# Optimization experiments

Measured on AMD Instinct MI355X. Metric: run time of the kernel, lower is better.

## Reference

```python
import jax, jax.numpy as jnp
import numpy as np

N, E, G = 2048, 4096, 128      # nodes, edges, graphs
H, IN, ED = 128, 11, 4         # hidden, input node feat, edge feat
BN_EPS = 1e-5


def setup_inputs() -> dict:
    key = jax.random.key(0)
    ks = iter(jax.random.split(key, 40))
    r = lambda shape, s=0.1: jax.random.normal(next(ks), shape, jnp.float32) * s
    inp = dict(
        x=r((N, IN), 1.0),
        edge_attr=jax.random.uniform(next(ks), (E, ED), jnp.float32),
        edge_index=jax.random.randint(next(ks), (2, E), 0, N).astype(jnp.int32),
        batch=jnp.sort(jax.random.randint(next(ks), (N,), 0, G)).astype(jnp.int32),
        # layer 0 (in=11 -> out=128)
        w1_0=r((ED, H)), b1_0=jnp.zeros(H), w2_0=r((H, IN * H), 0.02), b2_0=jnp.zeros(IN * H),
        root_0=r((IN, H)), bias_0=jnp.zeros(H),
        bn_g0=jnp.ones(H), bn_b0=jnp.zeros(H), bn_m0=r((H,), 0.1),
        bn_v0=jax.random.uniform(next(ks), (H,), jnp.float32, 0.5, 1.5),
        # layers 1..4 stacked (in=out=128)
        w1_s=r((4, ED, H)), b1_s=jnp.zeros((4, H)), w2_s=r((4, H, H * H), 0.02), b2_s=jnp.zeros((4, H * H)),
        root_s=r((4, H, H)), bias_s=jnp.zeros((4, H)),
        bn_gs=jnp.ones((4, H)), bn_bs=jnp.zeros((4, H)), bn_ms=r((4, H), 0.1),
        bn_vs=jax.random.uniform(next(ks), (4, H), jnp.float32, 0.5, 1.5),
        # readout MLP
        lin1_w=r((H, H // 2)), lin1_b=jnp.zeros(H // 2),
        lin2_w=r((H // 2, 1)), lin2_b=jnp.zeros(1),
    )
    return inp


def _nnconv(x, src, dst, edge_attr, w1, b1, w2, b2, root, bias):
    in_c = x.shape[-1]
    h = jax.nn.relu(edge_attr @ w1 + b1)                 # [E, H]
    w_e = (h @ w2 + b2).reshape(-1, in_c, H)             # [E, in, H] per-edge weight
    msg = jnp.einsum('ei,eio->eo', x[src], w_e)          # gather + per-edge matvec
    s = jax.ops.segment_sum(msg, dst, num_segments=N)
    cnt = jax.ops.segment_sum(jnp.ones(dst.shape, x.dtype), dst, num_segments=N)
    aggr = s / jnp.maximum(cnt, 1.0)[:, None]            # scatter-mean
    return aggr + x @ root + bias


def _bn_eval(x, g, b, m, v):
    return (x - m) * jax.lax.rsqrt(v + BN_EPS) * g + b


def reference(x, edge_attr, w1_0, b1_0, w2_0, b2_0, root_0, bias_0,
              bn_g0, bn_b0, bn_m0, bn_v0,
              w1_s, b1_s, w2_s, b2_s, root_s, bias_s,
              bn_gs, bn_bs, bn_ms, bn_vs,
              lin1_w, lin1_b, lin2_w, lin2_b,
              edge_index, batch):
    src, dst = edge_index[0], edge_index[1]
    # layer 0
    h = jax.nn.relu(_bn_eval(
        _nnconv(x, src, dst, edge_attr, w1_0, b1_0, w2_0, b2_0, root_0, bias_0),
        bn_g0, bn_b0, bn_m0, bn_v0))
    # layers 1..4 with residual (dims match)
    for l in range(4):
        h_new = jax.nn.relu(_bn_eval(
            _nnconv(h, src, dst, edge_attr, w1_s[l], b1_s[l], w2_s[l], b2_s[l], root_s[l], bias_s[l]),
            bn_gs[l], bn_bs[l], bn_ms[l], bn_vs[l]))
        h = h + h_new
    # global mean pool over graphs
    gs = jax.ops.segment_sum(h, batch, num_segments=G)
    gc = jax.ops.segment_sum(jnp.ones((N,), h.dtype), batch, num_segments=G)
    g = gs / jnp.maximum(gc, 1.0)[:, None]
    # readout (dropout is identity in eval mode)
    g = jax.nn.relu(g @ lin1_w + lin1_b)
    return g @ lin2_w + lin2_b
```

## Files before the change

### kernel.cpp

```cpp
#include <hip/hip_runtime.h>
#include <cstdint>
#include <cstddef>

#define NN 2048
#define NE 4096
#define NG 128
#define HD 128
#define SKM 16
#define SK0 5
#define NCH 64
#define CHE 64

typedef __attribute__((ext_vector_type(8))) _Float16 f16x8;
typedef __attribute__((ext_vector_type(4))) float f32x4;

#define GLOAD_LDS16(gptr, lptr)                                                          \
  __builtin_amdgcn_global_load_lds((const __attribute__((address_space(1))) unsigned int*)(gptr), \
                                   (__attribute__((address_space(3))) unsigned int*)(lptr), 16, 0, 0)

__global__ __launch_bounds__(256) void k_prep(
    const float* __restrict__ ea,
    const float* __restrict__ w1_0, const float* __restrict__ b1_0,
    const float* __restrict__ w1_s, const float* __restrict__ b1_s,
    const float* __restrict__ x,
    const float* __restrict__ w2_0, const float* __restrict__ b2_0,
    const float* __restrict__ w2s, const float* __restrict__ b2s,
    const int* __restrict__ dst, int* __restrict__ hist,
    _Float16* __restrict__ hb, _Float16* __restrict__ x16,
    _Float16* __restrict__ w2T0, _Float16* __restrict__ w2T) {
  __shared__ float s[64][65];
  const int bid = blockIdx.x, t = threadIdx.x;

  if (bid < 10240) {
    int idx = bid * 256 + t;
    int c = idx & (HD - 1);
    int e = (idx >> 7) & (NE - 1);
    int l = idx >> 19;
    const float* w1 = (l == 0) ? w1_0 : (w1_s + (size_t)(l - 1) * 4 * HD);
    const float* b1 = (l == 0) ? b1_0 : (b1_s + (size_t)(l - 1) * HD);
    float4 a = *(const float4*)(ea + (size_t)e * 4);
    float v = b1[c] + a.x * w1[c] + a.y * w1[HD + c] + a.z * w1[2 * HD + c] + a.w * w1[3 * HD + c];
    hb[idx] = (_Float16)fmaxf(v, 0.f);
  } else if (bid < 10368) {
    int idx = (bid - 10240) * 256 + t;
    int n = idx >> 4, i = idx & 15;
    x16[idx] = (_Float16)(i < 11 ? x[(size_t)n * 11 + i] : 0.f);
  } else if (bid < 10496) {
    int o = bid - 10368;
    for (int kap = t; kap < 2080; kap += 256) {
      int k = kap >> 4, i = kap & 15;
      float v = 0.f;
      if (i < 11) {
        if (k < 128) v = w2_0[(size_t)k * 1408 + i * 128 + o];
        else if (k == 128) v = b2_0[i * 128 + o];
      }
      w2T0[(size_t)o * 2080 + kap] = (_Float16)v;
    }
  } else if (bid < 12560) {
    int idx2 = bid - 10496;
    int l = idx2 / 516;
    int rem = idx2 - l * 516;
    int ob = rem / 258;
    int kb = rem - ob * 258;
    const float* w2 = w2s + (size_t)l * 16384 * 128;
    const float* b2 = b2s + (size_t)l * 128 * 128;
    _Float16* out = w2T + (size_t)l * 128 * 16512;
    int k0 = kb * 64, o0 = ob * 64;
    int r = t >> 4, c4 = (t & 15) * 4;
#pragma unroll
    for (int it = 0; it < 4; ++it) {
      int kk = k0 + r + it * 16;
      const float* srcp = (kk < 16384) ? (w2 + (size_t)kk * 128 + o0 + c4)
                                       : (b2 + (size_t)(kk - 16384) * 128 + o0 + c4);
      *(float4*)&s[r + it * 16][c4] = *(const float4*)srcp;
    }
    __syncthreads();
    int rr = t >> 3, c8 = (t & 7) * 8;
#pragma unroll
    for (int it = 0; it < 2; ++it) {
      int ol = rr + it * 32;
      _Float16 pk[8];
#pragma unroll
      for (int j = 0; j < 8; ++j) pk[j] = (_Float16)s[c8 + j][ol];
      *(f16x8*)(out + (size_t)(o0 + ol) * 16512 + k0 + c8) = *(const f16x8*)pk;
    }
  } else {
    int e = (bid - 12560) * 256 + t;
    if (e < NE) atomicAdd(&hist[(e >> 6) * NN + dst[e]], 1);
  }
}

__global__ __launch_bounds__(1024) void k_scan2(const int* __restrict__ hist,
                                                int* __restrict__ rowptr,
                                                int* __restrict__ chunkoff,
                                                const int* __restrict__ batch,
                                                int* __restrict__ gstart) {
  __shared__ int s[NN];
  int t = threadIdx.x;
  int c0 = 0, c1 = 0;
  for (int c = 0; c < NCH; ++c) { c0 += hist[c * NN + t]; c1 += hist[c * NN + t + 1024]; }
  s[t] = c0; s[t + 1024] = c1;
  __syncthreads();
  for (int d = 1; d < NN; d <<= 1) {
    int a0 = s[t], a1 = s[t + 1024];
    int v0 = (t >= d) ? s[t - d] : 0;
    int v1 = (t + 1024 >= d) ? s[t + 1024 - d] : 0;
    __syncthreads();
    s[t] = a0 + v0; s[t + 1024] = a1 + v1;
    __syncthreads();
  }
  rowptr[t + 1] = s[t]; rowptr[t + 1025] = s[t + 1024];
  if (t == 0) rowptr[0] = 0;
  int run0 = s[t] - c0, run1 = s[t + 1024] - c1;
  for (int c = 0; c < NCH; ++c) {
    chunkoff[c * NN + t] = run0;        run0 += hist[c * NN + t];
    chunkoff[c * NN + t + 1024] = run1; run1 += hist[c * NN + t + 1024];
  }
  if (t <= NG) {
    int lo = 0, hi = NN;
    while (lo < hi) { int mid = (lo + hi) >> 1; if (batch[mid] < t) lo = mid + 1; else hi = mid; }
    gstart[t] = lo;
  }
}

__global__ __launch_bounds__(64) void k_fill2(const int* __restrict__ dst,
                                              const int* __restrict__ chunkoff,
                                              int* __restrict__ elist) {
  __shared__ int sd[CHE];
  int c = blockIdx.x, t = threadIdx.x;
  int e = c * CHE + t;
  int dv = dst[e];
  sd[t] = dv;
  __syncthreads();
  int lrank = 0;
  for (int j = 0; j < t; ++j) lrank += (sd[j] == dv) ? 1 : 0;
  elist[chunkoff[c * NN + dv] + lrank] = e;
}

__global__ __launch_bounds__(256, 2) void k_mma0(
    const _Float16* __restrict__ xh,
    const _Float16* __restrict__ hb,
    const _Float16* __restrict__ w2T,
    const int* __restrict__ src,
    _Float16* __restrict__ msgp) {
  constexpr int KT = 2080;
  __shared__ _Float16 Bs[2][4096];
  __shared__ _Float16 hTl[26][128];

  const int tid = threadIdx.x;
  const int e0 = blockIdx.x * 128;
  const int w = tid >> 6, l = tid & 63, l16 = l & 15, g = l >> 4;

  const int k0 = blockIdx.y * 13, nk = 13;
  const int kb = k0 * 2;

  int nd[8];
#pragma unroll
  for (int mt = 0; mt < 8; ++mt) nd[mt] = src[e0 + mt * 16 + l16];

  for (int idx = tid; idx < 26 * 128; idx += 256) {
    int kk = idx >> 7, m = idx & 127;
    int k = kb + kk;
    _Float16 v;
    if (k < 128) v = hb[(size_t)(e0 + m) * 128 + k];
    else v = (k == 128) ? (_Float16)1.0f : (_Float16)0.0f;
    hTl[kk][m] = v;
  }

  f16x8 xr[8];
#pragma unroll
  for (int mt = 0; mt < 8; ++mt)
    xr[mt] = *(const f16x8*)(xh + (size_t)nd[mt] * 16 + (g & 1) * 8);

  auto stageB = [&](int buf, int c) {
    const int kap0 = c * 32;
#pragma unroll
    for (int j2 = 0; j2 < 2; ++j2) {
      int ntg = w * 2 + j2;
      const _Float16* gp = w2T + (size_t)(ntg * 16 + l16) * KT + kap0 + g * 8;
      GLOAD_LDS16(gp, &Bs[buf][(w * 128 + j2 * 64) * 8]);
    }
  };

  stageB(0, k0);
  __syncthreads();

  f32x4 acc[8][2];
#pragma unroll
  for (int mt = 0; mt < 8; ++mt)
#pragma unroll
    for (int jj = 0; jj < 2; ++jj) acc[mt][jj] = (f32x4){0.f, 0.f, 0.f, 0.f};

  int buf = 0;
  for (int j = 0; j < nk; ++j) {
    if (j + 1 < nk) {
      stageB(buf ^ 1, k0 + j + 1);
      asm volatile("s_waitcnt vmcnt(2)" ::: "memory");
    } else {
      asm volatile("s_waitcnt vmcnt(0)" ::: "memory");
    }
    __builtin_amdgcn_sched_barrier(0);

    f16x8 bv0 = *(const f16x8*)&Bs[buf][(size_t)(w * 2 + 0) * 512 + l * 8];
    f16x8 bv1 = *(const f16x8*)&Bs[buf][(size_t)(w * 2 + 1) * 512 + l * 8];
#pragma unroll
    for (int mt = 0; mt < 8; ++mt) {
      _Float16 hh = hTl[2 * j + (g >> 1)][mt * 16 + l16];
      f16x8 hv = {hh, hh, hh, hh, hh, hh, hh, hh};
      f16x8 av = xr[mt] * hv;
      acc[mt][0] = __builtin_amdgcn_mfma_f32_16x16x32_f16(av, bv0, acc[mt][0], 0, 0, 0);
      acc[mt][1] = __builtin_amdgcn_mfma_f32_16x16x32_f16(av, bv1, acc[mt][1], 0, 0, 0);
    }
    buf ^= 1;
    __syncthreads();
  }

  _Float16* mp = msgp + ((size_t)blockIdx.y * NE + e0) * 128;
#pragma unroll
  for (int mt = 0; mt < 8; ++mt)
#pragma unroll
    for (int jj = 0; jj < 2; ++jj)
#pragma unroll
      for (int r = 0; r < 4; ++r) {
        int row = mt * 16 + 4 * g + r;
        mp[(size_t)row * 128 + w * 32 + jj * 16 + l16] = (_Float16)acc[mt][jj][r];
      }
}

__global__ __launch_bounds__(512, 2) void k_mma3(
    const _Float16* __restrict__ xh,
    const _Float16* __restrict__ hb,
    const _Float16* __restrict__ w2T,
    const int* __restrict__ src,
    _Float16* __restrict__ msgp) {
  constexpr int KT = 16512;
  __shared__ __align__(16) _Float16 Bs[4][4096];
  __shared__ _Float16 hTl[9][256];

  const int tid = threadIdx.x;
  const int w = tid >> 6, l = tid & 63, l16 = l & 15, g = l >> 4;
  const int bid = blockIdx.x;
  const int eb = bid >> 4, sk = bid & 15;
  const int e0 = eb * 256;
  const int mg = w & 3, ng = w >> 2;

  int k0, nk;
  if (sk == 0) { k0 = 0; nk = 9; } else { k0 = 9 + (sk - 1) * 8; nk = 8; }
  const int nsteps = nk * 4;

  auto stageB = [&](int s) {
    const int jk = s >> 2, win = s & 3;
    const int kap0 = (k0 + jk) * 128 + win * 32;
    const _Float16* gp = w2T + (size_t)(w * 16 + l16) * KT + kap0 + g * 8;
    GLOAD_LDS16(gp, &Bs[s & 3][w * 512]);
  };

  stageB(0);
  stageB(1);

  int nd[4];
#pragma unroll
  for (int mt = 0; mt < 4; ++mt) nd[mt] = src[e0 + mg * 64 + mt * 16 + l16];
  f16x8 xw[4][4];
#pragma unroll
  for (int mt = 0; mt < 4; ++mt)
#pragma unroll
    for (int win = 0; win < 4; ++win)
      xw[mt][win] = *(const f16x8*)(xh + (size_t)nd[mt] * 128 + win * 32 + g * 8);

  for (int idx = tid; idx < nk * 256; idx += 512) {
    int jk = idx >> 8, m = idx & 255;
    int k = k0 + jk;
    hTl[jk][m] = (k < 128) ? hb[(size_t)(e0 + m) * 128 + k]
                           : (_Float16)(k == 128 ? 1.0f : 0.0f);
  }
  __syncthreads();

  f32x4 acc[4][4];
#pragma unroll
  for (int mt = 0; mt < 4; ++mt)
#pragma unroll
    for (int j2 = 0; j2 < 4; ++j2) acc[mt][j2] = (f32x4){0.f, 0.f, 0.f, 0.f};

  for (int jk = 0; jk < nk; ++jk) {
    _Float16 hv[4];
#pragma unroll
    for (int mt = 0; mt < 4; ++mt) hv[mt] = hTl[jk][mg * 64 + mt * 16 + l16];
#pragma unroll
    for (int win = 0; win < 4; ++win) {
      const int s = jk * 4 + win;
      if (s + 2 < nsteps) {
        stageB(s + 2);
        asm volatile("s_waitcnt vmcnt(2)" ::: "memory");
      } else if (s + 2 == nsteps) {
        asm volatile("s_waitcnt vmcnt(1)" ::: "memory");
      } else {
        asm volatile("s_waitcnt vmcnt(0)" ::: "memory");
      }
      __builtin_amdgcn_s_barrier();

      const _Float16* bp = &Bs[win][ng * 2048 + g * 128 + l16 * 8];
      f16x8 bv0 = *(const f16x8*)(bp);
      f16x8 bv1 = *(const f16x8*)(bp + 512);
      f16x8 bv2 = *(const f16x8*)(bp + 1024);
      f16x8 bv3 = *(const f16x8*)(bp + 1536);
#pragma unroll
      for (int mt = 0; mt < 4; ++mt) {
        _Float16 hh = hv[mt];
        f16x8 hs = {hh, hh, hh, hh, hh, hh, hh, hh};
        f16x8 av = xw[mt][win] * hs;
        acc[mt][0] = __builtin_amdgcn_mfma_f32_16x16x32_f16(av, bv0, acc[mt][0], 0, 0, 0);
        acc[mt][1] = __builtin_amdgcn_mfma_f32_16x16x32_f16(av, bv1, acc[mt][1], 0, 0, 0);
        acc[mt][2] = __builtin_amdgcn_mfma_f32_16x16x32_f16(av, bv2, acc[mt][2], 0, 0, 0);
        acc[mt][3] = __builtin_amdgcn_mfma_f32_16x16x32_f16(av, bv3, acc[mt][3], 0, 0, 0);
      }
    }
  }

  _Float16* mp = msgp + ((size_t)sk * NE + e0) * 128;
#pragma unroll
  for (int mt = 0; mt < 4; ++mt)
#pragma unroll
    for (int j2 = 0; j2 < 4; ++j2)
#pragma unroll
      for (int r = 0; r < 4; ++r) {
        int row = mg * 64 + mt * 16 + 4 * g + r;
        int col = (ng * 4 + j2) * 16 + l16;
        mp[(size_t)row * 128 + col] = (_Float16)acc[mt][j2][r];
      }
}

template <int INR, int NSK>
__global__ void k_au(const _Float16* __restrict__ msgp, const int* __restrict__ rowptr,
                     const int* __restrict__ elist, const float* __restrict__ xin,
                     const float* __restrict__ root, const float* __restrict__ bias,
                     const float* __restrict__ bg, const float* __restrict__ bb,
                     const float* __restrict__ bm, const float* __restrict__ bv,
                     const float* __restrict__ h_prev, float* __restrict__ h_out,
                     _Float16* __restrict__ h_out_h) {
  int n = blockIdx.x, t = threadIdx.x;
  __shared__ float xr[INR];
  if (t < INR) xr[t] = xin[(size_t)n * INR + t];
  int beg = rowptr[n], end = rowptr[n + 1];
  float v = 0.f;
  for (int j = beg; j < end; ++j) {
    int e = elist[j];
#pragma unroll
    for (int s = 0; s < NSK; ++s) v += (float)msgp[((size_t)s * NE + e) * HD + t];
  }
  v /= fmaxf((float)(end - beg), 1.f);
  __syncthreads();
  float acc = v + bias[t];
#pragma unroll 8
  for (int k = 0; k < INR; ++k) acc += xr[k] * root[(size_t)k * HD + t];
  float bn = (acc - bm[t]) * rsqrtf(bv[t] + 1e-5f) * bg[t] + bb[t];
  float r = fmaxf(bn, 0.f);
  float val = h_prev ? (h_prev[(size_t)n * HD + t] + r) : r;
  h_out[(size_t)n * HD + t] = val;
  h_out_h[(size_t)n * HD + t] = (_Float16)val;
}

__global__ void k_poolread(const float* __restrict__ h, const int* __restrict__ gstart,
                           const float* __restrict__ w1, const float* __restrict__ b1,
                           const float* __restrict__ w2, const float* __restrict__ b2,
                           float* __restrict__ out) {
  int g = blockIdx.x, t = threadIdx.x;
  __shared__ float row[HD];
  int beg = gstart[g], end = gstart[g + 1];
  float v = 0.f;
  for (int n = beg; n < end; ++n) v += h[(size_t)n * HD + t];
  row[t] = v / fmaxf((float)(end - beg), 1.f);
  __syncthreads();
  if (t < 64) {
    float acc = b1[t];
#pragma unroll 8
    for (int k = 0; k < HD; ++k) acc += row[k] * w1[(size_t)k * 64 + t];
    float vv = fmaxf(acc, 0.f) * w2[t];
#pragma unroll
    for (int off = 32; off > 0; off >>= 1) vv += __shfl_down(vv, off);
    if (t == 0) out[g] = vv + b2[0];
  }
}

extern "C" void kernel_launch(void* const* d_in, const int* in_sizes, int n_in,
                              void* d_out, int out_size, void* d_ws, size_t ws_size,
                              hipStream_t stream) {
  const float* x      = (const float*)d_in[0];
  const float* ea     = (const float*)d_in[1];
  const int*   eidx   = (const int*)d_in[2];
  const int*   batch  = (const int*)d_in[3];
  const float* w1_0   = (const float*)d_in[4];
  const float* b1_0   = (const float*)d_in[5];
  const float* w2_0   = (const float*)d_in[6];
  const float* b2_0   = (const float*)d_in[7];
  const float* root_0 = (const float*)d_in[8];
  const float* bias_0 = (const float*)d_in[9];
  const float* bn_g0  = (const float*)d_in[10];
  const float* bn_b0  = (const float*)d_in[11];
  const float* bn_m0  = (const float*)d_in[12];
  const float* bn_v0  = (const float*)d_in[13];
  const float* w1_s   = (const float*)d_in[14];
  const float* b1_s   = (const float*)d_in[15];
  const float* w2_s   = (const float*)d_in[16];
  const float* b2_s   = (const float*)d_in[17];
  const float* root_s = (const float*)d_in[18];
  const float* bias_s = (const float*)d_in[19];
  const float* bn_gs  = (const float*)d_in[20];
  const float* bn_bs  = (const float*)d_in[21];
  const float* bn_ms  = (const float*)d_in[22];
  const float* bn_vs  = (const float*)d_in[23];
  const float* lin1_w = (const float*)d_in[24];
  const float* lin1_b = (const float*)d_in[25];
  const float* lin2_w = (const float*)d_in[26];
  const float* lin2_b = (const float*)d_in[27];
  float* out = (float*)d_out;

  char* wsb = (char*)d_ws;
  size_t off = 0;
  auto alloc = [&](size_t bytes) { void* p = wsb + off; off = (off + bytes + 255) & ~(size_t)255; return p; };
  int*      rowptr   = (int*)alloc((NN + 4) * 4);
  int*      elist    = (int*)alloc(NE * 4);
  int*      gstart   = (int*)alloc((NG + 4) * 4);
  int*      hist     = (int*)alloc((size_t)NCH * NN * 4);
  int*      chunkoff = (int*)alloc((size_t)NCH * NN * 4);
  _Float16* hbf      = (_Float16*)alloc((size_t)5 * NE * HD * 2);
  _Float16* x16      = (_Float16*)alloc((size_t)NN * 16 * 2);
  _Float16* w2T0     = (_Float16*)alloc((size_t)128 * 2080 * 2);
  _Float16* w2T      = (_Float16*)alloc((size_t)4 * 128 * 16512 * 2);
  float*    hnA      = (float*)alloc((size_t)NN * HD * 4);
  float*    hnB      = (float*)alloc((size_t)NN * HD * 4);
  _Float16* hnAh     = (_Float16*)alloc((size_t)NN * HD * 2);
  _Float16* hnBh     = (_Float16*)alloc((size_t)NN * HD * 2);
  _Float16* msgp     = (_Float16*)alloc((size_t)SKM * NE * HD * 2);

  const int* src = eidx;
  const int* dstp = eidx + NE;

  hipMemsetAsync(hist, 0, (size_t)NCH * NN * 4, stream);
  k_prep<<<dim3(12576), 256, 0, stream>>>(ea, w1_0, b1_0, w1_s, b1_s, x,
                                          w2_0, b2_0, w2_s, b2_s,
                                          dstp, hist, hbf, x16, w2T0, w2T);
  k_scan2<<<1, 1024, 0, stream>>>(hist, rowptr, chunkoff, batch, gstart);
  k_fill2<<<dim3(NCH), 64, 0, stream>>>(dstp, chunkoff, elist);

  k_mma0<<<dim3(NE / 128, SK0), 256, 0, stream>>>(x16, hbf, w2T0, src, msgp);
  k_au<11, SK0><<<NN, HD, 0, stream>>>(msgp, rowptr, elist, x, root_0, bias_0,
                                       bn_g0, bn_b0, bn_m0, bn_v0, nullptr, hnA, hnAh);

  float* cur = hnA;  _Float16* curh = hnAh;
  float* nxt = hnB;  _Float16* nxth = hnBh;
  for (int l = 1; l <= 4; ++l) {
    const _Float16* w2Tl = w2T + (size_t)(l - 1) * 128 * 16512;
    k_mma3<<<dim3(256), 512, 0, stream>>>(curh, hbf + (size_t)l * NE * HD, w2Tl, src, msgp);
    k_au<128, SKM><<<NN, HD, 0, stream>>>(msgp, rowptr, elist, cur,
                                          root_s + (size_t)(l - 1) * HD * HD,
                                          bias_s + (size_t)(l - 1) * HD,
                                          bn_gs + (size_t)(l - 1) * HD, bn_bs + (size_t)(l - 1) * HD,
                                          bn_ms + (size_t)(l - 1) * HD, bn_vs + (size_t)(l - 1) * HD,
                                          cur, nxt, nxth);
    float* tf = cur; cur = nxt; nxt = tf;
    _Float16* th = curh; curh = nxth; nxth = th;
  }

  k_poolread<<<NG, HD, 0, stream>>>(cur, gstart, lin1_w, lin1_b, lin2_w, lin2_b, out);
}
```

Measured before the change: 237.3 us.

## Pre-swizzle per-layer edge weights into MFMA fragment order and restructure aggregation

Rewrites the prep transpose so the layer weights are stored in a fragment-ready layout, one contiguous block per split-K slice. k_mma3 can then load B operands straight from global memory into registers with a two-deep register prefetch, instead of staging them through LDS with barriers. The warp tiling changes from 4x2 to 2x4, each wave covering 128 rows and 32 columns. Separately, the aggregation kernel now handles four nodes per 256-thread block and splits the root matvec across four accumulators, and scan reads per-node counts filled by a second atomic instead of summing 64 histogram chunks. Dropping the LDS staging removes shared-memory traffic and barriers, but B loads become exposed global latency and the extra atomics add contention.

```diff
diff --git a/kernel.cpp b/kernel.cpp
--- a/kernel.cpp
+++ b/kernel.cpp
@@ -10,6 +10,7 @@
 #define SK0 5
 #define NCH 64
 #define CHE 64
+#define WSTRIDE (40 * 4096)
 
 typedef __attribute__((ext_vector_type(8))) _Float16 f16x8;
 typedef __attribute__((ext_vector_type(4))) float f32x4;
@@ -25,10 +26,10 @@
     const float* __restrict__ x,
     const float* __restrict__ w2_0, const float* __restrict__ b2_0,
     const float* __restrict__ w2s, const float* __restrict__ b2s,
-    const int* __restrict__ dst, int* __restrict__ hist,
+    const int* __restrict__ dst, int* __restrict__ hist, int* __restrict__ counts,
     _Float16* __restrict__ hb, _Float16* __restrict__ x16,
-    _Float16* __restrict__ w2T0, _Float16* __restrict__ w2T) {
-  __shared__ float s[64][65];
+    _Float16* __restrict__ w2T0, _Float16* __restrict__ w2F) {
+  __shared__ float sld[32][128];
   const int bid = blockIdx.x, t = threadIdx.x;
 
   if (bid < 10240) {
@@ -59,46 +60,55 @@
   } else if (bid < 12560) {
     int idx2 = bid - 10496;
     int l = idx2 / 516;
-    int rem = idx2 - l * 516;
-    int ob = rem / 258;
-    int kb = rem - ob * 258;
-    const float* w2 = w2s + (size_t)l * 16384 * 128;
-    const float* b2 = b2s + (size_t)l * 128 * 128;
-    _Float16* out = w2T + (size_t)l * 128 * 16512;
-    int k0 = kb * 64, o0 = ob * 64;
-    int r = t >> 4, c4 = (t & 15) * 4;
-#pragma unroll
-    for (int it = 0; it < 4; ++it) {
-      int kk = k0 + r + it * 16;
-      const float* srcp = (kk < 16384) ? (w2 + (size_t)kk * 128 + o0 + c4)
-                                       : (b2 + (size_t)(kk - 16384) * 128 + o0 + c4);
-      *(float4*)&s[r + it * 16][c4] = *(const float4*)srcp;
-    }
+    int r = idx2 - l * 516;
+    int sk, s;
+    if (r < 36) { sk = 0; s = r; } else { sk = 1 + (r - 36) / 32; s = (r - 36) & 31; }
+    int nk = (sk == 0) ? 9 : 8;
+    int k0 = (sk == 0) ? 0 : 9 + (sk - 1) * 8;
+    int wp = s / (2 * nk);
+    int rem = s - wp * 2 * nk;
+    int jk = rem >> 1, wv = rem & 1;
+    int k = k0 + jk;
+    int ib = (wp * 2 + wv) * 32;
+    const float* srcb = (k < 128)
+        ? (w2s + ((size_t)l * 16384 + (size_t)k * 128 + ib) * 128)
+        : (b2s + ((size_t)l * 128 + ib) * 128);
+    float* sf = &sld[0][0];
+#pragma unroll
+    for (int q = 0; q < 4; ++q)
+      *(float4*)&sf[t * 16 + q * 4] = *(const float4*)&srcb[t * 16 + q * 4];
     __syncthreads();
-    int rr = t >> 3, c8 = (t & 7) * 8;
-#pragma unroll
-    for (int it = 0; it < 2; ++it) {
-      int ol = rr + it * 32;
+    _Float16* outp = w2F + (((size_t)l * 16 + sk) * (size_t)WSTRIDE) + (size_t)s * 4096;
+#pragma unroll
+    for (int j2 = 0; j2 < 2; ++j2) {
+      int f = j2 * 2048 + t * 8;
+      int ng = f >> 10, nt = (f >> 9) & 1, lane = (f >> 3) & 63;
+      int g = lane >> 4, l16 = lane & 15;
+      int o = ng * 32 + nt * 16 + l16;
       _Float16 pk[8];
 #pragma unroll
-      for (int j = 0; j < 8; ++j) pk[j] = (_Float16)s[c8 + j][ol];
-      *(f16x8*)(out + (size_t)(o0 + ol) * 16512 + k0 + c8) = *(const f16x8*)pk;
+      for (int j = 0; j < 8; ++j) pk[j] = (_Float16)sld[g * 8 + j][o];
+      *(f16x8*)(outp + f) = *(const f16x8*)pk;
     }
   } else {
     int e = (bid - 12560) * 256 + t;
-    if (e < NE) atomicAdd(&hist[(e >> 6) * NN + dst[e]], 1);
+    if (e < NE) {
+      int d = dst[e];
+      atomicAdd(&hist[(e >> 6) * NN + d], 1);
+      atomicAdd(&counts[d], 1);
+    }
   }
 }
 
 __global__ __launch_bounds__(1024) void k_scan2(const int* __restrict__ hist,
+                                                const int* __restrict__ counts,
                                                 int* __restrict__ rowptr,
                                                 int* __restrict__ chunkoff,
                                                 const int* __restrict__ batch,
                                                 int* __restrict__ gstart) {
   __shared__ int s[NN];
   int t = threadIdx.x;
-  int c0 = 0, c1 = 0;
-  for (int c = 0; c < NCH; ++c) { c0 += hist[c * NN + t]; c1 += hist[c * NN + t + 1024]; }
+  int c0 = counts[t], c1 = counts[t + 1024];
   s[t] = c0; s[t + 1024] = c1;
   __syncthreads();
   for (int d = 1; d < NN; d <<= 1) {
@@ -230,134 +240,159 @@
 __global__ __launch_bounds__(512, 2) void k_mma3(
     const _Float16* __restrict__ xh,
     const _Float16* __restrict__ hb,
-    const _Float16* __restrict__ w2T,
+    const _Float16* __restrict__ w2Fl,
     const int* __restrict__ src,
     _Float16* __restrict__ msgp) {
-  constexpr int KT = 16512;
-  __shared__ __align__(16) _Float16 Bs[4][4096];
-  __shared__ _Float16 hTl[9][256];
+  __shared__ _Float16 h_lds[256][10];
 
   const int tid = threadIdx.x;
   const int w = tid >> 6, l = tid & 63, l16 = l & 15, g = l >> 4;
+  const int mg = w >> 2, ng = w & 3;
   const int bid = blockIdx.x;
   const int eb = bid >> 4, sk = bid & 15;
   const int e0 = eb * 256;
-  const int mg = w & 3, ng = w >> 2;
-
-  int k0, nk;
-  if (sk == 0) { k0 = 0; nk = 9; } else { k0 = 9 + (sk - 1) * 8; nk = 8; }
-  const int nsteps = nk * 4;
-
-  auto stageB = [&](int s) {
-    const int jk = s >> 2, win = s & 3;
-    const int kap0 = (k0 + jk) * 128 + win * 32;
-    const _Float16* gp = w2T + (size_t)(w * 16 + l16) * KT + kap0 + g * 8;
-    GLOAD_LDS16(gp, &Bs[s & 3][w * 512]);
-  };
-
-  stageB(0);
-  stageB(1);
-
-  int nd[4];
-#pragma unroll
-  for (int mt = 0; mt < 4; ++mt) nd[mt] = src[e0 + mg * 64 + mt * 16 + l16];
-  f16x8 xw[4][4];
-#pragma unroll
-  for (int mt = 0; mt < 4; ++mt)
-#pragma unroll
-    for (int win = 0; win < 4; ++win)
-      xw[mt][win] = *(const f16x8*)(xh + (size_t)nd[mt] * 128 + win * 32 + g * 8);
-
-  for (int idx = tid; idx < nk * 256; idx += 512) {
-    int jk = idx >> 8, m = idx & 255;
-    int k = k0 + jk;
-    hTl[jk][m] = (k < 128) ? hb[(size_t)(e0 + m) * 128 + k]
-                           : (_Float16)(k == 128 ? 1.0f : 0.0f);
-  }
+
+  const int nk = (sk == 0) ? 9 : 8;
+  const int k0 = (sk == 0) ? 0 : 9 + (sk - 1) * 8;
+
+  for (int i = tid; i < (nk << 8); i += 512) {
+    int kk = i >> 8, m = i & 255;
+    int k = k0 + kk;
+    h_lds[m][kk] = (k < 128) ? hb[(size_t)(e0 + m) * 128 + k] : (_Float16)1.0f;
+  }
+
+  int nd[8];
+#pragma unroll
+  for (int mt = 0; mt < 8; ++mt) nd[mt] = src[e0 + mg * 128 + mt * 16 + l16];
   __syncthreads();
 
-  f32x4 acc[4][4];
-#pragma unroll
-  for (int mt = 0; mt < 4; ++mt)
-#pragma unroll
-    for (int j2 = 0; j2 < 4; ++j2) acc[mt][j2] = (f32x4){0.f, 0.f, 0.f, 0.f};
-
-  for (int jk = 0; jk < nk; ++jk) {
-    _Float16 hv[4];
-#pragma unroll
-    for (int mt = 0; mt < 4; ++mt) hv[mt] = hTl[jk][mg * 64 + mt * 16 + l16];
-#pragma unroll
-    for (int win = 0; win < 4; ++win) {
-      const int s = jk * 4 + win;
-      if (s + 2 < nsteps) {
-        stageB(s + 2);
-        asm volatile("s_waitcnt vmcnt(2)" ::: "memory");
-      } else if (s + 2 == nsteps) {
-        asm volatile("s_waitcnt vmcnt(1)" ::: "memory");
-      } else {
-        asm volatile("s_waitcnt vmcnt(0)" ::: "memory");
+  const _Float16* bw = w2Fl + (size_t)sk * WSTRIDE + ng * 1024 + (size_t)l * 8;
+
+  f32x4 acc[8][2];
+#pragma unroll
+  for (int mt = 0; mt < 8; ++mt) {
+    acc[mt][0] = (f32x4){0.f, 0.f, 0.f, 0.f};
+    acc[mt][1] = (f32x4){0.f, 0.f, 0.f, 0.f};
+  }
+
+#define LOAD4(v0, v1, v2, v3, pairidx)                                   \
+  {                                                                      \
+    const _Float16* q_ = bw + (size_t)(pairidx) * 8192;                  \
+    v0 = *(const f16x8*)(q_);                                            \
+    v1 = *(const f16x8*)(q_ + 512);                                      \
+    v2 = *(const f16x8*)(q_ + 4096);                                     \
+    v3 = *(const f16x8*)(q_ + 4608);                                     \
+  }
+
+#define BODY(jk_, b0, b1, b2, b3)                                        \
+  {                                                                      \
+    _Float16 hv_[8];                                                     \
+    _Pragma("unroll")                                                    \
+    for (int mt = 0; mt < 8; ++mt)                                       \
+      hv_[mt] = h_lds[mg * 128 + mt * 16 + l16][jk_];                    \
+    _Pragma("unroll")                                                    \
+    for (int mt = 0; mt < 8; ++mt) {                                     \
+      _Float16 hh = hv_[mt];                                             \
+      f16x8 hs = {hh, hh, hh, hh, hh, hh, hh, hh};                       \
+      f16x8 av = xw0[mt] * hs;                                           \
+      acc[mt][0] = __builtin_amdgcn_mfma_f32_16x16x32_f16(av, b0, acc[mt][0], 0, 0, 0); \
+      acc[mt][1] = __builtin_amdgcn_mfma_f32_16x16x32_f16(av, b1, acc[mt][1], 0, 0, 0); \
+    }                                                                    \
+    _Pragma("unroll")                                                    \
+    for (int mt = 0; mt < 8; ++mt) {                                     \
+      _Float16 hh = hv_[mt];                                             \
+      f16x8 hs = {hh, hh, hh, hh, hh, hh, hh, hh};                       \
+      f16x8 av = xw1[mt] * hs;                                           \
+      acc[mt][0] = __builtin_amdgcn_mfma_f32_16x16x32_f16(av, b2, acc[mt][0], 0, 0, 0); \
+      acc[mt][1] = __builtin_amdgcn_mfma_f32_16x16x32_f16(av, b3, acc[mt][1], 0, 0, 0); \
+    }                                                                    \
+  }
+
+  for (int wp = 0; wp < 2; ++wp) {
+    f16x8 xw0[8], xw1[8];
+#pragma unroll
+    for (int mt = 0; mt < 8; ++mt) {
+      const _Float16* xp = xh + (size_t)nd[mt] * 128 + (wp * 2) * 32 + g * 8;
+      xw0[mt] = *(const f16x8*)(xp);
+      xw1[mt] = *(const f16x8*)(xp + 32);
+    }
+    const int pb = wp * nk;
+    f16x8 c0, c1, c2, c3, n0, n1, n2, n3;
+    LOAD4(c0, c1, c2, c3, pb);
+    int jk = 0;
+    while (true) {
+      LOAD4(n0, n1, n2, n3, pb + jk + 1);
+      BODY(jk, c0, c1, c2, c3);
+      ++jk;
+      if (jk >= nk) break;
+      LOAD4(c0, c1, c2, c3, pb + jk + 1);
+      BODY(jk, n0, n1, n2, n3);
+      ++jk;
+      if (jk >= nk) break;
+    }
+  }
+#undef LOAD4
+#undef BODY
+
+  _Float16* mp = msgp + ((size_t)sk * NE + e0) * 128;
+#pragma unroll
+  for (int mt = 0; mt < 8; ++mt)
+#pragma unroll
+    for (int nt = 0; nt < 2; ++nt)
+#pragma unroll
+      for (int r = 0; r < 4; ++r) {
+        int row = mg * 128 + mt * 16 + 4 * g + r;
+        int col = ng * 32 + nt * 16 + l16;
+        mp[(size_t)row * 128 + col] = (_Float16)acc[mt][nt][r];
       }
-      __builtin_amdgcn_s_barrier();
-
-      const _Float16* bp = &Bs[win][ng * 2048 + g * 128 + l16 * 8];
-      f16x8 bv0 = *(const f16x8*)(bp);
-      f16x8 bv1 = *(const f16x8*)(bp + 512);
-      f16x8 bv2 = *(const f16x8*)(bp + 1024);
-      f16x8 bv3 = *(const f16x8*)(bp + 1536);
-#pragma unroll
-      for (int mt = 0; mt < 4; ++mt) {
-        _Float16 hh = hv[mt];
-        f16x8 hs = {hh, hh, hh, hh, hh, hh, hh, hh};
-        f16x8 av = xw[mt][win] * hs;
-        acc[mt][0] = __builtin_amdgcn_mfma_f32_16x16x32_f16(av, bv0, acc[mt][0], 0, 0, 0);
-        acc[mt][1] = __builtin_amdgcn_mfma_f32_16x16x32_f16(av, bv1, acc[mt][1], 0, 0, 0);
-        acc[mt][2] = __builtin_amdgcn_mfma_f32_16x16x32_f16(av, bv2, acc[mt][2], 0, 0, 0);
-        acc[mt][3] = __builtin_amdgcn_mfma_f32_16x16x32_f16(av, bv3, acc[mt][3], 0, 0, 0);
+}
+
+template <int INR, int NSK, bool RES>
+__global__ __launch_bounds__(256) void k_au2(
+    const _Float16* __restrict__ msgp, const int* __restrict__ rowptr,
+    const int* __restrict__ elist, const float* __restrict__ xin,
+    const float* __restrict__ root, const float* __restrict__ bias,
+    const float* __restrict__ bg, const float* __restrict__ bb,
+    const float* __restrict__ bm, const float* __restrict__ bv,
+    const float* __restrict__ h_prev, float* __restrict__ h_out,
+    _Float16* __restrict__ h_out_h) {
+  __shared__ float xr[2][INR];
+  const int nb = blockIdx.x;
+  const int sub = threadIdx.x >> 7, col = threadIdx.x & 127;
+  for (int p = 0; p < 2; ++p) {
+    int n = nb * 4 + p * 2 + sub;
+    if (col < INR) xr[sub][col] = xin[(size_t)n * INR + col];
+    __syncthreads();
+    int beg = rowptr[n], end = rowptr[n + 1];
+    float v = 0.f;
+    for (int j = beg; j < end; ++j) {
+      int e = elist[j];
+#pragma unroll
+      for (int s = 0; s < NSK; ++s) v += (float)msgp[((size_t)s * NE + e) * HD + col];
+    }
+    v /= fmaxf((float)(end - beg), 1.f);
+    float acc = v + bias[col];
+    if constexpr (INR == 128) {
+      float a0 = 0.f, a1 = 0.f, a2 = 0.f, a3 = 0.f;
+#pragma unroll 4
+      for (int k = 0; k < 128; k += 4) {
+        a0 += xr[sub][k + 0] * root[(size_t)(k + 0) * HD + col];
+        a1 += xr[sub][k + 1] * root[(size_t)(k + 1) * HD + col];
+        a2 += xr[sub][k + 2] * root[(size_t)(k + 2) * HD + col];
+        a3 += xr[sub][k + 3] * root[(size_t)(k + 3) * HD + col];
       }
-    }
-  }
-
-  _Float16* mp = msgp + ((size_t)sk * NE + e0) * 128;
-#pragma unroll
-  for (int mt = 0; mt < 4; ++mt)
-#pragma unroll
-    for (int j2 = 0; j2 < 4; ++j2)
-#pragma unroll
-      for (int r = 0; r < 4; ++r) {
-        int row = mg * 64 + mt * 16 + 4 * g + r;
-        int col = (ng * 4 + j2) * 16 + l16;
-        mp[(size_t)row * 128 + col] = (_Float16)acc[mt][j2][r];
-      }
-}
-
-template <int INR, int NSK>
-__global__ void k_au(const _Float16* __restrict__ msgp, const int* __restrict__ rowptr,
-                     const int* __restrict__ elist, const float* __restrict__ xin,
-                     const float* __restrict__ root, const float* __restrict__ bias,
-                     const float* __restrict__ bg, const float* __restrict__ bb,
-                     const float* __restrict__ bm, const float* __restrict__ bv,
-                     const float* __restrict__ h_prev, float* __restrict__ h_out,
-                     _Float16* __restrict__ h_out_h) {
-  int n = blockIdx.x, t = threadIdx.x;
-  __shared__ float xr[INR];
-  if (t < INR) xr[t] = xin[(size_t)n * INR + t];
-  int beg = rowptr[n], end = rowptr[n + 1];
-  float v = 0.f;
-  for (int j = beg; j < end; ++j) {
-    int e = elist[j];
-#pragma unroll
-    for (int s = 0; s < NSK; ++s) v += (float)msgp[((size_t)s * NE + e) * HD + t];
-  }
-  v /= fmaxf((float)(end - beg), 1.f);
-  __syncthreads();
-  float acc = v + bias[t];
-#pragma unroll 8
-  for (int k = 0; k < INR; ++k) acc += xr[k] * root[(size_t)k * HD + t];
-  float bn = (acc - bm[t]) * rsqrtf(bv[t] + 1e-5f) * bg[t] + bb[t];
-  float r = fmaxf(bn, 0.f);
-  float val = h_prev ? (h_prev[(size_t)n * HD + t] + r) : r;
-  h_out[(size_t)n * HD + t] = val;
-  h_out_h[(size_t)n * HD + t] = (_Float16)val;
+      acc += (a0 + a1) + (a2 + a3);
+    } else {
+#pragma unroll
+      for (int k = 0; k < INR; ++k) acc += xr[sub][k] * root[(size_t)k * HD + col];
+    }
+    float bn = (acc - bm[col]) * rsqrtf(bv[col] + 1e-5f) * bg[col] + bb[col];
+    float r = fmaxf(bn, 0.f);
+    float val = RES ? (h_prev[(size_t)n * HD + col] + r) : r;
+    h_out[(size_t)n * HD + col] = val;
+    h_out_h[(size_t)n * HD + col] = (_Float16)val;
+    __syncthreads();
+  }
 }
 
 __global__ void k_poolread(const float* __restrict__ h, const int* __restrict__ gstart,
@@ -418,15 +453,16 @@
   char* wsb = (char*)d_ws;
   size_t off = 0;
   auto alloc = [&](size_t bytes) { void* p = wsb + off; off = (off + bytes + 255) & ~(size_t)255; return p; };
+  int*      hist     = (int*)alloc((size_t)NCH * NN * 4);
+  int*      counts   = (int*)alloc(NN * 4);
   int*      rowptr   = (int*)alloc((NN + 4) * 4);
   int*      elist    = (int*)alloc(NE * 4);
   int*      gstart   = (int*)alloc((NG + 4) * 4);
-  int*      hist     = (int*)alloc((size_t)NCH * NN * 4);
   int*      chunkoff = (int*)alloc((size_t)NCH * NN * 4);
   _Float16* hbf      = (_Float16*)alloc((size_t)5 * NE * HD * 2);
   _Float16* x16      = (_Float16*)alloc((size_t)NN * 16 * 2);
   _Float16* w2T0     = (_Float16*)alloc((size_t)128 * 2080 * 2);
-  _Float16* w2T      = (_Float16*)alloc((size_t)4 * 128 * 16512 * 2);
+  _Float16* w2F      = (_Float16*)alloc((size_t)4 * 16 * WSTRIDE * 2);
   float*    hnA      = (float*)alloc((size_t)NN * HD * 4);
   float*    hnB      = (float*)alloc((size_t)NN * HD * 4);
   _Float16* hnAh     = (_Float16*)alloc((size_t)NN * HD * 2);
@@ -436,28 +472,29 @@
   const int* src = eidx;
   const int* dstp = eidx + NE;
 
-  hipMemsetAsync(hist, 0, (size_t)NCH * NN * 4, stream);
+  hipMemsetAsync(hist, 0, ((size_t)NCH * NN + NN) * 4, stream);
   k_prep<<<dim3(12576), 256, 0, stream>>>(ea, w1_0, b1_0, w1_s, b1_s, x,
                                           w2_0, b2_0, w2_s, b2_s,
-                                          dstp, hist, hbf, x16, w2T0, w2T);
-  k_scan2<<<1, 1024, 0, stream>>>(hist, rowptr, chunkoff, batch, gstart);
+                                          dstp, hist, counts, hbf, x16, w2T0, w2F);
+  k_scan2<<<1, 1024, 0, stream>>>(hist, counts, rowptr, chunkoff, batch, gstart);
   k_fill2<<<dim3(NCH), 64, 0, stream>>>(dstp, chunkoff, elist);
 
   k_mma0<<<dim3(NE / 128, SK0), 256, 0, stream>>>(x16, hbf, w2T0, src, msgp);
-  k_au<11, SK0><<<NN, HD, 0, stream>>>(msgp, rowptr, elist, x, root_0, bias_0,
-                                       bn_g0, bn_b0, bn_m0, bn_v0, nullptr, hnA, hnAh);
+  k_au2<11, SK0, false><<<dim3(512), 256, 0, stream>>>(msgp, rowptr, elist, x, root_0, bias_0,
+                                                       bn_g0, bn_b0, bn_m0, bn_v0,
+                                                       nullptr, hnA, hnAh);
 
   float* cur = hnA;  _Float16* curh = hnAh;
   float* nxt = hnB;  _Float16* nxth = hnBh;
   for (int l = 1; l <= 4; ++l) {
-    const _Float16* w2Tl = w2T + (size_t)(l - 1) * 128 * 16512;
-    k_mma3<<<dim3(256), 512, 0, stream>>>(curh, hbf + (size_t)l * NE * HD, w2Tl, src, msgp);
-    k_au<128, SKM><<<NN, HD, 0, stream>>>(msgp, rowptr, elist, cur,
-                                          root_s + (size_t)(l - 1) * HD * HD,
-                                          bias_s + (size_t)(l - 1) * HD,
-                                          bn_gs + (size_t)(l - 1) * HD, bn_bs + (size_t)(l - 1) * HD,
-                                          bn_ms + (size_t)(l - 1) * HD, bn_vs + (size_t)(l - 1) * HD,
-                                          cur, nxt, nxth);
+    const _Float16* w2Fl = w2F + (size_t)(l - 1) * 16 * WSTRIDE;
+    k_mma3<<<dim3(256), 512, 0, stream>>>(curh, hbf + (size_t)l * NE * HD, w2Fl, src, msgp);
+    k_au2<128, SKM, true><<<dim3(512), 256, 0, stream>>>(
+        msgp, rowptr, elist, cur,
+        root_s + (size_t)(l - 1) * HD * HD, bias_s + (size_t)(l - 1) * HD,
+        bn_gs + (size_t)(l - 1) * HD, bn_bs + (size_t)(l - 1) * HD,
+        bn_ms + (size_t)(l - 1) * HD, bn_vs + (size_t)(l - 1) * HD,
+        cur, nxt, nxth);
     float* tf = cur; cur = nxt; nxt = tf;
     _Float16* th = curh; curh = nxth; nxth = th;
   }
```

New measurement: 263.1 us. +10.9%, slower.
